# Kernel optimization log

Hardware: AMD Instinct MI355X
Metric: run time of the kernel (lower is better)

## Reference

```python
import jax, jax.numpy as jnp
import numpy as np

B, N, D = 128, 64, 20
H, WM = 256, 4
CAUG = D + 1                      # time-augmented path channels
SIG = CAUG + CAUG * (CAUG - 1) // 2   # depth-2 log-signature channels = 231
C = SIG + 1                       # time-augmented control channels = 232
EPS = 1e-5


def _ln(x, g, b):
    m = jnp.mean(x, -1, keepdims=True)
    v = jnp.var(x, -1, keepdims=True)
    return (x - m) * jax.lax.rsqrt(v + EPS) * g + b


def setup_inputs():
    key = jax.random.key(0)
    ks = jax.random.split(key, 12)
    w = lambda k, s: (jax.random.normal(k, s) * 0.02).astype(jnp.float32)
    z = lambda s: jnp.zeros(s, jnp.float32)
    o = lambda s: jnp.ones(s, jnp.float32)
    return dict(
        x=jax.random.normal(ks[0], (B, N, D), jnp.float32),
        hW1=w(ks[1], (D, H)), hb1=z(H), hW2=w(ks[2], (H, H)), hb2=z(H),
        fW1=w(ks[3], (H, WM * H)), fb1=z(WM * H), g1=o(WM * H), be1=z(WM * H),
        fW2=w(ks[4], (WM * H, H)), fb2=z(H), g2=o(H), be2=z(H),
        fW3=w(ks[5], (H, H)), fb3=z(H),
        fW4=w(ks[6], (H, H * C)), fb4=z(H * C),
        yW1=w(ks[7], (H, H // 2)), yb1=z(H // 2), yW2=w(ks[8], (H // 2, 1)), yb2=z(1),
        zW1=w(ks[9], (H, H)), zb1=z(H), zW2=w(ks[10], (H, D)), zb2=z(D),
        sg=o(SIG), sb=z(SIG),
    )


def _forward(x, hW1, hb1, hW2, hb2, fW1, fb1, g1, be1, fW2, fb2, g2, be2,
             fW3, fb3, fW4, fb4, yW1, yb1, yW2, yb2, zW1, zb1, zW2, zb2, sg, sb):
    t = jnp.linspace(0.0, 1.0, N).astype(x.dtype)
    # --- depth-2 streamed log-signature of time-augmented path, basepoint 0 ---
    p = jnp.concatenate([jnp.broadcast_to(t[None, :, None], (B, N, 1)), x], -1)  # (B,N,CAUG)
    prev = jnp.concatenate([jnp.zeros((B, 1, CAUG), x.dtype), p[:, :-1]], 1)
    d = p - prev                                          # piecewise-linear segment increments
    term = prev[..., :, None] * d[..., None, :] - d[..., :, None] * prev[..., None, :]
    levy = 0.5 * jnp.cumsum(term, axis=1)                 # Levy areas, (B,N,CAUG,CAUG)
    iu, ju = np.triu_indices(CAUG, 1)
    logsig = jnp.concatenate([p, levy[:, :, iu, ju]], -1)  # level-1 + level-2 log-sig, (B,N,SIG)
    logsig = _ln(logsig, sg, sb)                          # sig_norm
    # --- natural cubic spline of time-augmented control ---
    y = jnp.concatenate([jnp.broadcast_to(t[None, :, None], (B, N, 1)), logsig], -1)  # (B,N,C)
    h = 1.0 / (N - 1)
    A = np.zeros((N, N), np.float32)
    A[0, 0] = A[-1, -1] = 1.0
    for i in range(1, N - 1):
        A[i, i - 1] = h / 6.0
        A[i, i] = 2.0 * h / 3.0
        A[i, i + 1] = h / 6.0
    rhs = jnp.concatenate([jnp.zeros((B, 1, C), y.dtype),
                           (y[:, 2:] - 2.0 * y[:, 1:-1] + y[:, :-2]) / h,
                           jnp.zeros((B, 1, C), y.dtype)], 1)
    M = jnp.linalg.solve(jnp.asarray(A), rhs.transpose(1, 0, 2).reshape(N, B * C))
    M = M.reshape(N, B, C).transpose(1, 0, 2)             # natural-spline second derivatives
    dy = (y[:, 1:] - y[:, :-1]) / h
    d_knot = dy - (h / 6.0) * (2.0 * M[:, :-1] + M[:, 1:])   # dX/dt at left knots, (B,N-1,C)
    d_mid = dy + (h / 24.0) * (M[:, :-1] - M[:, 1:])         # dX/dt at segment midpoints
    # --- initial hidden state ---
    h0 = jax.nn.relu(x[:, 0] @ hW1 + hb1) @ hW2 + hb2

    def vf(zz):  # RDEFunc MLP -> (B,H,C)
        a = jax.nn.relu(_ln(zz @ fW1 + fb1, g1, be1))
        a = jax.nn.relu(_ln(a @ fW2 + fb2, g2, be2))
        a = jax.nn.relu(a @ fW3 + fb3)
        return (a @ fW4 + fb4).reshape(B, H, C)

    def g(zz, dX):
        return jnp.einsum('bhc,bc->bh', vf(zz), dX)

    def step(zz, dd):  # explicit midpoint step of dz = F(z) dX/dt dt
        dk, dm = dd
        k1 = g(zz, dk)
        zn = zz + h * g(zz + 0.5 * h * k1, dm)
        return zn, zn

    _, hs = jax.lax.scan(step, h0, (d_knot.transpose(1, 0, 2), d_mid.transpose(1, 0, 2)))
    hT = hs[-1]                                            # terminal hidden (return_path=False)
    Y = jax.nn.relu(hT @ yW1 + yb1) @ yW2 + yb2
    Z = jax.nn.relu(hT @ zW1 + zb1) @ zW2 + zb2
    return Y, Z, hT


def reference(x, hW1, hb1, hW2, hb2, fW1, fb1, g1, be1, fW2, fb2, g2, be2,
              fW3, fb3, fW4, fb4, yW1, yb1, yW2, yb2, zW1, zb1, zW2, zb2, sg, sb):
    return _forward(x, hW1, hb1, hW2, hb2, fW1, fb1, g1, be1, fW2, fb2, g2, be2,
                    fW3, fb3, fW4, fb4, yW1, yb1, yW2, yb2, zW1, zb1, zW2, zb2, sg, sb)
```

## Files before the change

### kernel.cpp

```cpp
#include <hip/hip_runtime.h>

#define B 128
#define N 64
#define D 20
#define H 256
#define WMH 1024
#define CAUG 21
#define SIG 231
#define C 232
#define CP 240
#define KA 288
#define NSEG 63
#define NPH 126
#define HSTEP (1.0f/63.0f)
#define EPS 1e-5f

typedef __attribute__((ext_vector_type(8))) short short8;
typedef __attribute__((ext_vector_type(4))) float f32x4;
typedef __attribute__((ext_vector_type(4))) unsigned int uint4v;
typedef __attribute__((ext_vector_type(2))) int int2v;
typedef __attribute__((ext_vector_type(4))) int int4v;
typedef unsigned int uint;

__device__ inline short f2bf(float f) {
  uint u = __float_as_uint(f);
  uint r = (u + 0x7fffu + ((u >> 16) & 1u)) >> 16;
  return (short)r;
}
__device__ inline float bf2f(short h) {
  return __uint_as_float(((uint)(unsigned short)h) << 16);
}
#define MFMA16(a, b, c) __builtin_amdgcn_mfma_f32_16x16x32_bf16((a), (b), (c), 0, 0, 0)

__device__ inline void cstoreu(uint* p, uint v) {
  __hip_atomic_store(p, v, __ATOMIC_RELAXED, __HIP_MEMORY_SCOPE_AGENT);
}
__device__ inline void cstoref(float* p, float v) {
  __hip_atomic_store(p, v, __ATOMIC_RELAXED, __HIP_MEMORY_SCOPE_AGENT);
}
__device__ inline void cstorei(int* p, int v) {
  __hip_atomic_store(p, v, __ATOMIC_RELAXED, __HIP_MEMORY_SCOPE_AGENT);
}

#define CLOAD8(r0,r1,r2,r3,r4,r5,r6,r7,addr)                                   \
  asm volatile("global_load_dwordx4 %0, %8, off sc0 sc1\n\t"                   \
               "global_load_dwordx4 %1, %8, off offset:16 sc0 sc1\n\t"         \
               "global_load_dwordx4 %2, %8, off offset:128 sc0 sc1\n\t"        \
               "global_load_dwordx4 %3, %8, off offset:144 sc0 sc1\n\t"        \
               "global_load_dwordx4 %4, %8, off offset:256 sc0 sc1\n\t"        \
               "global_load_dwordx4 %5, %8, off offset:272 sc0 sc1\n\t"        \
               "global_load_dwordx4 %6, %8, off offset:384 sc0 sc1\n\t"        \
               "global_load_dwordx4 %7, %8, off offset:400 sc0 sc1\n\t"        \
               "s_waitcnt vmcnt(0)"                                            \
               : "=&v"(r0), "=&v"(r1), "=&v"(r2), "=&v"(r3),                   \
                 "=&v"(r4), "=&v"(r5), "=&v"(r6), "=&v"(r7)                    \
               : "v"(addr)                                                     \
               : "memory")

#define CLOAD2(r0,r1,addr)                                                     \
  asm volatile("global_load_dwordx4 %0, %2, off sc0 sc1\n\t"                   \
               "global_load_dwordx4 %1, %2, off offset:16 sc0 sc1\n\t"         \
               "s_waitcnt vmcnt(0)"                                            \
               : "=&v"(r0), "=&v"(r1) : "v"(addr) : "memory")

#define CLOAD9(r0,r1,r2,r3,r4,r5,r6,r7,r8,a0,a1,a2,a3,a4,a5,a6,a7,a8)          \
  asm volatile("global_load_dwordx4 %0, %9, off sc0 sc1\n\t"                   \
               "global_load_dwordx4 %1, %10, off sc0 sc1\n\t"                  \
               "global_load_dwordx4 %2, %11, off sc0 sc1\n\t"                  \
               "global_load_dwordx4 %3, %12, off sc0 sc1\n\t"                  \
               "global_load_dwordx4 %4, %13, off sc0 sc1\n\t"                  \
               "global_load_dwordx4 %5, %14, off sc0 sc1\n\t"                  \
               "global_load_dwordx4 %6, %15, off sc0 sc1\n\t"                  \
               "global_load_dwordx4 %7, %16, off sc0 sc1\n\t"                  \
               "global_load_dwordx4 %8, %17, off sc0 sc1\n\t"                  \
               "s_waitcnt vmcnt(0)"                                            \
               : "=&v"(r0), "=&v"(r1), "=&v"(r2), "=&v"(r3), "=&v"(r4),        \
                 "=&v"(r5), "=&v"(r6), "=&v"(r7), "=&v"(r8)                    \
               : "v"(a0), "v"(a1), "v"(a2), "v"(a3), "v"(a4), "v"(a5),         \
                 "v"(a6), "v"(a7), "v"(a8)                                     \
               : "memory")

__device__ inline void post(int* w, int v) {
  __builtin_amdgcn_fence(__ATOMIC_RELEASE, "workgroup");
  __syncthreads();
  if (threadIdx.x == 0) cstorei(w, v);
}
__device__ inline void poll16(const int* f, int tgt) {
  if (threadIdx.x < 64) {
    const int* p = f + (threadIdx.x & 15);
    for (;;) {
      int v;
      asm volatile("global_load_dword %0, %1, off sc0 sc1\n\ts_waitcnt vmcnt(0)"
                   : "=v"(v) : "v"(p) : "memory");
      if (__all(v >= tgt)) break;
      __builtin_amdgcn_s_sleep(1);
    }
  }
  __builtin_amdgcn_fence(__ATOMIC_ACQUIRE, "workgroup");
  __syncthreads();
}
__device__ inline void poll128(const int* f, int tgt) {
  if (threadIdx.x < 64) {
    const int* p = f + threadIdx.x * 2;
    for (;;) {
      int2v v;
      asm volatile("global_load_dwordx2 %0, %1, off sc0 sc1\n\ts_waitcnt vmcnt(0)"
                   : "=v"(v) : "v"(p) : "memory");
      if (__all(v[0] >= tgt && v[1] >= tgt)) break;
      __builtin_amdgcn_s_sleep(1);
    }
  }
  __builtin_amdgcn_fence(__ATOMIC_ACQUIRE, "workgroup");
  __syncthreads();
}
__device__ inline void poll256(const int* f, int tgt) {
  if (threadIdx.x < 64) {
    const int* p = f + threadIdx.x * 4;
    for (;;) {
      int4v v;
      asm volatile("global_load_dwordx4 %0, %1, off sc0 sc1\n\ts_waitcnt vmcnt(0)"
                   : "=v"(v) : "v"(p) : "memory");
      if (__all(v[0] >= tgt && v[1] >= tgt && v[2] >= tgt && v[3] >= tgt)) break;
      __builtin_amdgcn_s_sleep(1);
    }
  }
  __builtin_amdgcn_fence(__ATOMIC_ACQUIRE, "workgroup");
  __syncthreads();
}

__device__ inline void unpk(uint4v a, uint4v b, short8& ah, short8& al) {
#pragma unroll
  for (int e = 0; e < 4; e++) {
    ah[e]     = (short)(a[e] >> 16); al[e]     = (short)(a[e] & 0xffffu);
    ah[4 + e] = (short)(b[e] >> 16); al[4 + e] = (short)(b[e] & 0xffffu);
  }
}

__global__ __launch_bounds__(256) void k_logsig(const float* __restrict__ x,
                                                const float* __restrict__ sg,
                                                const float* __restrict__ sb,
                                                float* __restrict__ y) {
  __shared__ float yb[N][C];
  int b = blockIdx.x, tid = threadIdx.x;
  for (int ii = tid; ii < N * CAUG; ii += 256) {
    int n = ii / CAUG, j = ii % CAUG;
    float v = (j == 0) ? (n * (1.0f / 63.0f)) : x[(b * N + n) * D + (j - 1)];
    yb[n][1 + j] = v;
  }
  __syncthreads();
  if (tid < 210) {
    int i = 0, rem = tid;
    while (rem >= (CAUG - 1) - i) { rem -= (CAUG - 1) - i; i++; }
    int j = i + 1 + rem;
    float acc = 0.f, pi_prev = 0.f, pj_prev = 0.f;
    for (int n = 0; n < N; n++) {
      float pi = yb[n][1 + i], pj = yb[n][1 + j];
      float di = pi - pi_prev, dj = pj - pj_prev;
      acc += 0.5f * (pi_prev * dj - di * pj_prev);
      yb[n][1 + CAUG + tid] = acc;
      pi_prev = pi; pj_prev = pj;
    }
  }
  __syncthreads();
  int w = tid >> 6, l = tid & 63;
  for (int n = w; n < N; n += 4) {
    float s1 = 0.f, s2 = 0.f;
    for (int s = l; s < SIG; s += 64) { float v = yb[n][1 + s]; s1 += v; s2 += v * v; }
    for (int off = 32; off > 0; off >>= 1) { s1 += __shfl_down(s1, off); s2 += __shfl_down(s2, off); }
    s1 = __shfl(s1, 0); s2 = __shfl(s2, 0);
    float mean = s1 * (1.0f / SIG);
    float var  = s2 * (1.0f / SIG) - mean * mean;
    float rs = rsqrtf(var + EPS);
    float* yrow = y + ((size_t)b * N + n) * C;
    if (l == 0) yrow[0] = n * (1.0f / 63.0f);
    for (int s = l; s < SIG; s += 64)
      yrow[1 + s] = (yb[n][1 + s] - mean) * rs * sg[s] + sb[s];
  }
}

__global__ __launch_bounds__(256) void k_spline(const float* __restrict__ y,
                                                float* __restrict__ dknot,
                                                float* __restrict__ dmid) {
  __shared__ float yb[N * C];
  __shared__ float cp_s[62], id_s[62];
  int b = blockIdx.x, tid = threadIdx.x;
  for (int ii = tid; ii < N * C; ii += 256) yb[ii] = y[(size_t)b * N * C + ii];
  if (tid == 0) {
    const float a = HSTEP / 6.f, bb = 2.f * HSTEP / 3.f;
    float id0 = 1.f / bb; id_s[0] = id0; cp_s[0] = a * id0;
    for (int j = 1; j < 62; j++) {
      float den = bb - a * cp_s[j - 1];
      float idj = 1.f / den; id_s[j] = idj; cp_s[j] = a * idj;
    }
  }
  __syncthreads();
  int c = tid;
  if (c >= 232 && c < CP) {
    for (int n = 0; n < NSEG; n++) {
      dknot[((size_t)n * B + b) * CP + c] = 0.f;
      dmid [((size_t)n * B + b) * CP + c] = 0.f;
    }
  } else if (c < 232) {
    const float a = HSTEP / 6.f;
    float dp[62];
    dp[0] = (yb[2 * C + c] - 2.f * yb[1 * C + c] + yb[0 * C + c]) * 63.0f * id_s[0];
#pragma unroll
    for (int j = 1; j < 62; j++) {
      float rj = (yb[(j + 2) * C + c] - 2.f * yb[(j + 1) * C + c] + yb[j * C + c]) * 63.0f;
      dp[j] = (rj - a * dp[j - 1]) * id_s[j];
    }
#pragma unroll
    for (int j = 60; j >= 0; j--) dp[j] -= cp_s[j] * dp[j + 1];
#pragma unroll
    for (int n = 0; n < NSEG; n++) {
      float Mn  = (n == 0)  ? 0.f : dp[n - 1];
      float Mn1 = (n == 62) ? 0.f : dp[n];
      float dy = (yb[(n + 1) * C + c] - yb[n * C + c]) * 63.0f;
      dknot[((size_t)n * B + b) * CP + c] = dy - (HSTEP / 6.f)  * (2.f * Mn + Mn1);
      dmid [((size_t)n * B + b) * CP + c] = dy + (HSTEP / 24.f) * (Mn - Mn1);
    }
  }
}

__global__ __launch_bounds__(256) void k_h0(const float* __restrict__ x,
                                            const float* __restrict__ hW1,
                                            const float* __restrict__ hb1,
                                            const float* __restrict__ hW2,
                                            const float* __restrict__ hb2,
                                            float* __restrict__ z,
                                            uint* __restrict__ Xu) {
  __shared__ float r[H];
  int b = blockIdx.x, tid = threadIdx.x;
  float s = hb1[tid];
#pragma unroll
  for (int d = 0; d < D; d++) s += x[(size_t)(b * N) * D + d] * hW1[d * H + tid];
  r[tid] = fmaxf(s, 0.f);
  __syncthreads();
  float s2 = hb2[tid];
  for (int k = 0; k < H; k++) s2 += r[k] * hW2[k * H + tid];
  z[b * H + tid] = s2;
  short hi = f2bf(s2);
  short lo = f2bf(s2 - bf2f(hi));
  Xu[b * H + tid] = ((uint)(unsigned short)hi << 16) | (unsigned short)lo;
}

__global__ __launch_bounds__(256) void k_prep_t(const float* __restrict__ fW4,
                                                short* __restrict__ W4T) {
  __shared__ float tile[64][65];
  int m0 = blockIdx.x * 64, k0 = blockIdx.y * 64;
  int lane = threadIdx.x & 63, wr = threadIdx.x >> 6;
#pragma unroll
  for (int j = 0; j < 16; j++) {
    int kk = wr * 16 + j;
    tile[kk][lane] = fW4[(size_t)(k0 + kk) * 59392 + m0 + lane];
  }
  __syncthreads();
#pragma unroll
  for (int j = 0; j < 16; j++) {
    int mloc = wr * 16 + j;
    int m = m0 + mloc;
    int hh = m / 232, cc = m - hh * 232;
    W4T[((size_t)hh * CP + cc) * KA + k0 + lane] = f2bf(tile[lane][mloc]);
  }
}

__global__ __launch_bounds__(256) void k_prep_pad(const float* __restrict__ fb4,
                                                  short* __restrict__ W4T) {
  int idx = blockIdx.x * 256 + threadIdx.x;
  const int partA = 61440 * 32;
  if (idx < partA) {
    int row = idx >> 5, j = idx & 31;
    int hh = row / CP, cc = row - hh * CP;
    short v = 0;
    if (j == 0 && cc < 232) v = f2bf(fb4[hh * 232 + cc]);
    W4T[(size_t)row * KA + 256 + j] = v;
  } else {
    int t = idx - partA;
    int k = t & 255; t >>= 8;
    int cc = 232 + (t & 7); int hh = t >> 3;
    W4T[((size_t)hh * CP + cc) * KA + k] = 0;
  }
}

__global__ __launch_bounds__(256) void k_prep_wt(const float* __restrict__ in,
                                                 short* __restrict__ out,
                                                 int K, int Nn) {
  __shared__ float tile[64][65];
  int n0 = blockIdx.x * 64, k0 = blockIdx.y * 64;
  int lane = threadIdx.x & 63, wr = threadIdx.x >> 6;
#pragma unroll
  for (int j = 0; j < 16; j++) {
    int kk = wr * 16 + j;
    tile[kk][lane] = in[(size_t)(k0 + kk) * Nn + n0 + lane];
  }
  __syncthreads();
#pragma unroll
  for (int j = 0; j < 16; j++) {
    int nl = wr * 16 + j;
    out[(size_t)(n0 + nl) * K + k0 + lane] = f2bf(tile[lane][nl]);
  }
}

__global__ __launch_bounds__(128) void k_prep_t3pad(short* __restrict__ t3aug) {
  int r = threadIdx.x;
  if (r < 128) {
    int base = ((r >> 4) * 9 + 8) * 64 + (r & 15);
#pragma unroll
    for (int q = 0; q < 4; q++)
#pragma unroll
      for (int j = 0; j < 8; j++)
        t3aug[(size_t)(base + q * 16) * 8 + j] = (q == 0 && j == 0) ? (short)0x3F80 : (short)0;
  }
}

__global__ __launch_bounds__(256) void k_prep_zero(int* __restrict__ p, int n) {
  int i = blockIdx.x * 256 + threadIdx.x;
  if (i < n) p[i] = 0;
}

__global__ __launch_bounds__(512, 1) void k_scan(
    const short* __restrict__ W1T, const float* __restrict__ fb1,
    const float* __restrict__ g1,  const float* __restrict__ be1,
    const short* __restrict__ W2T, const float* __restrict__ fb2,
    const float* __restrict__ g2,  const float* __restrict__ be2,
    const short* __restrict__ W3T, const float* __restrict__ fb3,
    const short* __restrict__ W4T,
    const float* __restrict__ dknot, const float* __restrict__ dmid,
    float* __restrict__ z, uint* __restrict__ Xu, uint* __restrict__ t3u,
    float* __restrict__ T1, float* __restrict__ T2,
    int* __restrict__ flags) {
  const int blk = blockIdx.x;
  const int tid = threadIdx.x;
  const int wave = tid >> 6, lane = tid & 63;
  const int lm = lane & 15, q = lane >> 4;
  const int m = (blk & 127) >> 4;
  const int n = blk & 15;
  const int ks = wave >> 2, nwt = wave & 3;

  __shared__ short t3s[B * KA];
  __shared__ float red2[8][256];
  __shared__ float red4[8][128];
  __shared__ float zcol[128];
  __shared__ float g1s[WMH], be1s[WMH];
  __shared__ float g2s[H], be2s[H];
  __shared__ float fb1s[64];
  __shared__ float fb2s[16], fb3s[16];

  int* eS1 = flags;
  int* eS2 = flags + 128;
  int* eS3 = flags + 256;
  int* eS4 = flags + 384;

  const int nts = (wave < 7) ? 2 : 1;
  const int nt0 = wave * 2;
  short8 bfr[2][9];
  for (int t = 0; t < nts; t++) {
    const short* wp = W4T + ((size_t)blk * CP + (nt0 + t) * 16 + lm) * KA + q * 8;
#pragma unroll
    for (int kc = 0; kc < 9; kc++)
      bfr[t][kc] = *(const short8*)(wp + kc * 32);
  }
  short8 w1f[4], w2f[4], w3f;
  if (blk < 128) {
    const short* p1 = W1T + ((size_t)(n * 64 + nwt * 16 + lm)) * H + ks * 128 + q * 8;
#pragma unroll
    for (int kc = 0; kc < 4; kc++) w1f[kc] = *(const short8*)(p1 + kc * 32);
    const short* p2 = W2T + ((size_t)(n * 16 + lm)) * WMH + wave * 128 + q * 8;
#pragma unroll
    for (int kc = 0; kc < 4; kc++) w2f[kc] = *(const short8*)(p2 + kc * 32);
    w3f = *(const short8*)(W3T + ((size_t)(n * 16 + lm)) * H + wave * 32 + q * 8);
  }
  for (int i = tid; i < WMH; i += 512) { g1s[i] = g1[i]; be1s[i] = be1[i]; }
  for (int i = tid; i < H; i += 512)   { g2s[i] = g2[i]; be2s[i] = be2[i]; }
  if (tid < 64) fb1s[tid] = fb1[n * 64 + tid];
  if (tid < 16) { fb2s[tid] = fb2[n * 16 + tid]; fb3s[tid] = fb3[n * 16 + tid]; }
  if (tid < 128) zcol[tid] = z[(size_t)tid * H + blk];
  __syncthreads();

#pragma unroll 1
  for (int p = 0; p < NPH; p++) {
    const int seg = p >> 1, pm = p & 1;
    const float* dX = (pm ? dmid : dknot) + (size_t)seg * B * CP;
    const float scale = pm ? HSTEP : 0.5f * HSTEP;

    if (blk < 128) {
      if (p) poll256(eS4, p);
      const uint* xp = Xu + (size_t)(m * 16 + lm) * H + ks * 128 + q * 8;
      uint4v xv[8];
      CLOAD8(xv[0], xv[1], xv[2], xv[3], xv[4], xv[5], xv[6], xv[7], xp);
      {
        f32x4 acc = {0.f, 0.f, 0.f, 0.f};
#pragma unroll
        for (int kc = 0; kc < 4; kc++) {
          short8 ah, al;
          unpk(xv[kc * 2], xv[kc * 2 + 1], ah, al);
          acc = MFMA16(ah, w1f[kc], acc);
          acc = MFMA16(al, w1f[kc], acc);
        }
#pragma unroll
        for (int r = 0; r < 4; r++) red2[wave][(q * 4 + r) * 16 + lm] = acc[r];
      }
      __syncthreads();
      if (wave < 4) {
        int col = n * 64 + wave * 16 + lm;
        float fb = fb1s[wave * 16 + lm];
#pragma unroll
        for (int r = 0; r < 4; r++) {
          int idx = (q * 4 + r) * 16 + lm;
          float v = red2[wave][idx] + red2[wave + 4][idx] + fb;
          cstoref(T1 + (size_t)(m * 16 + q * 4 + r) * WMH + col, v);
        }
      }
      post(eS1 + m * 16 + n, p + 1);

      poll16(eS1 + m * 16, p + 1);
      const float* tp = T1 + (size_t)(m * 16 + lm) * WMH + wave * 128 + q * 8;
      uint4v yv[8];
      CLOAD8(yv[0], yv[1], yv[2], yv[3], yv[4], yv[5], yv[6], yv[7], tp);
      {
        float s = 0.f, ss = 0.f;
#pragma unroll
        for (int i = 0; i < 8; i++)
#pragma unroll
          for (int e = 0; e < 4; e++) {
            float v = __uint_as_float(yv[i][e]);
            s += v; ss += v * v;
          }
        s += __shfl_xor(s, 16); ss += __shfl_xor(ss, 16);
        s += __shfl_xor(s, 32); ss += __shfl_xor(ss, 32);
        if (q == 0) { red2[wave][lm] = s; red2[wave][16 + lm] = ss; }
        __syncthreads();
        float S = 0.f, SS = 0.f;
#pragma unroll
        for (int w = 0; w < 8; w++) { S += red2[w][lm]; SS += red2[w][16 + lm]; }
        float mean = S * (1.f / WMH);
        float var  = SS * (1.f / WMH) - mean * mean;
        float rsv  = rsqrtf(var + EPS);
        __syncthreads();
        f32x4 acc = {0.f, 0.f, 0.f, 0.f};
#pragma unroll
        for (int kc = 0; kc < 4; kc++) {
          int kg = wave * 128 + kc * 32 + q * 8;
          short8 ah, al;
#pragma unroll
          for (int jj = 0; jj < 8; jj++) {
            float v = __uint_as_float(yv[kc * 2 + (jj >> 2)][jj & 3]);
            float a = fmaxf((v - mean) * rsv * g1s[kg + jj] + be1s[kg + jj], 0.f);
            short hi = f2bf(a);
            ah[jj] = hi;
            al[jj] = f2bf(a - bf2f(hi));
          }
          acc = MFMA16(ah, w2f[kc], acc);
          acc = MFMA16(al, w2f[kc], acc);
        }
#pragma unroll
        for (int r = 0; r < 4; r++) red2[wave][(q * 4 + r) * 16 + lm] = acc[r];
      }
      __syncthreads();
      if (tid < 256) {
        int ri = tid >> 4, ci = tid & 15;
        float v = fb2s[ci];
#pragma unroll
        for (int w = 0; w < 8; w++) v += red2[w][tid];
        cstoref(T2 + (size_t)(m * 16 + ri) * H + n * 16 + ci, v);
      }
      post(eS2 + m * 16 + n, p + 1);

      poll16(eS2 + m * 16, p + 1);
      const float* t2p = T2 + (size_t)(m * 16 + lm) * H + wave * 32 + q * 8;
      uint4v u0, u1;
      CLOAD2(u0, u1, t2p);
      {
        float s = 0.f, ss = 0.f;
#pragma unroll
        for (int e = 0; e < 4; e++) {
          float v0 = __uint_as_float(u0[e]), v1 = __uint_as_float(u1[e]);
          s += v0 + v1; ss += v0 * v0 + v1 * v1;
        }
        s += __shfl_xor(s, 16); ss += __shfl_xor(ss, 16);
        s += __shfl_xor(s, 32); ss += __shfl_xor(ss, 32);
        if (q == 0) { red2[wave][lm] = s; red2[wave][16 + lm] = ss; }
        __syncthreads();
        float S = 0.f, SS = 0.f;
#pragma unroll
        for (int w = 0; w < 8; w++) { S += red2[w][lm]; SS += red2[w][16 + lm]; }
        float mean = S * (1.f / H);
        float var  = SS * (1.f / H) - mean * mean;
        float rsv  = rsqrtf(var + EPS);
        __syncthreads();
        int kg = wave * 32 + q * 8;
        short8 ah, al;
#pragma unroll
        for (int jj = 0; jj < 8; jj++) {
          float v = __uint_as_float((jj < 4 ? u0[jj & 3] : u1[jj & 3]));
          float a = fmaxf((v - mean) * rsv * g2s[kg + jj] + be2s[kg + jj], 0.f);
          short hi = f2bf(a);
          ah[jj] = hi;
          al[jj] = f2bf(a - bf2f(hi));
        }
        f32x4 acc = {0.f, 0.f, 0.f, 0.f};
        acc = MFMA16(ah, w3f, acc);
        acc = MFMA16(al, w3f, acc);
#pragma unroll
        for (int r = 0; r < 4; r++) red2[wave][(q * 4 + r) * 16 + lm] = acc[r];
      }
      __syncthreads();
      if (tid < 256) {
        int ri = tid >> 4, ci = tid & 15;
        float v = fb3s[ci];
#pragma unroll
        for (int w = 0; w < 8; w++) v += red2[w][tid];
        v = fmaxf(v, 0.f);
        float vo = __shfl_xor(v, 1);
        if ((ci & 1) == 0) {
          int kglob = n * 16 + ci;
          int d = (m * 9 + (kglob >> 5)) * 64 + ((kglob >> 3) & 3) * 16 + ri;
          uint u = ((uint)(unsigned short)f2bf(vo) << 16)
                 | (unsigned short)f2bf(v);
          cstoreu(t3u + d * 4 + ((kglob & 7) >> 1), u);
        }
      }
      post(eS3 + m * 16 + n, p + 1);
    }

    {
      poll128(eS3, p + 1);
      {
        const uint* tb = t3u + tid * 4;
        uint4v r0, r1, r2, r3, r4, r5, r6, r7, r8;
        CLOAD9(r0, r1, r2, r3, r4, r5, r6, r7, r8,
               tb, tb + 2048, tb + 4096, tb + 6144, tb + 8192,
               tb + 10240, tb + 12288, tb + 14336, tb + 16384);
        *(uint4v*)(t3s + (size_t)(0 * 2048 + tid * 4) * 2) = r0;
        *(uint4v*)(t3s + (size_t)(1 * 2048 + tid * 4) * 2) = r1;
        *(uint4v*)(t3s + (size_t)(2 * 2048 + tid * 4) * 2) = r2;
        *(uint4v*)(t3s + (size_t)(3 * 2048 + tid * 4) * 2) = r3;
        *(uint4v*)(t3s + (size_t)(4 * 2048 + tid * 4) * 2) = r4;
        *(uint4v*)(t3s + (size_t)(5 * 2048 + tid * 4) * 2) = r5;
        *(uint4v*)(t3s + (size_t)(6 * 2048 + tid * 4) * 2) = r6;
        *(uint4v*)(t3s + (size_t)(7 * 2048 + tid * 4) * 2) = r7;
        *(uint4v*)(t3s + (size_t)(8 * 2048 + tid * 4) * 2) = r8;
      }
      __syncthreads();
      for (int mm = 0; mm < 8; mm++) {
        short8 afr[9];
#pragma unroll
        for (int kc = 0; kc < 9; kc++)
          afr[kc] = *(const short8*)(t3s + (size_t)((mm * 9 + kc) * 64 + lane) * 8);
        f32x4 acc0 = {0.f, 0.f, 0.f, 0.f}, acc1 = {0.f, 0.f, 0.f, 0.f};
#pragma unroll
        for (int kc = 0; kc < 9; kc++) {
          acc0 = MFMA16(afr[kc], bfr[0][kc], acc0);
          if (nts > 1) acc1 = MFMA16(afr[kc], bfr[1][kc], acc1);
        }
        float part[4];
#pragma unroll
        for (int r = 0; r < 4; r++) {
          int row = mm * 16 + q * 4 + r;
          float pv = acc0[r] * dX[(size_t)row * CP + nt0 * 16 + lm];
          if (nts > 1) pv += acc1[r] * dX[(size_t)row * CP + (nt0 + 1) * 16 + lm];
          part[r] = pv;
        }
#pragma unroll
        for (int r = 0; r < 4; r++) {
          part[r] += __shfl_xor(part[r], 1);
          part[r] += __shfl_xor(part[r], 2);
          part[r] += __shfl_xor(part[r], 4);
          part[r] += __shfl_xor(part[r], 8);
        }
        if (lm == 0) {
#pragma unroll
          for (int r = 0; r < 4; r++) red4[wave][mm * 16 + q * 4 + r] = part[r];
        }
      }
      __syncthreads();
      if (tid < 128) {
        int row = tid;
        float s = 0.f;
#pragma unroll
        for (int w = 0; w < 8; w++) s += red4[w][row];
        float zo = zcol[row] + scale * s;
        if (pm) zcol[row] = zo;
        if (p == NPH - 1) z[(size_t)row * H + blk] = zo;
        short hi = f2bf(zo);
        short lo = f2bf(zo - bf2f(hi));
        cstoreu(Xu + (size_t)row * H + blk,
                ((uint)(unsigned short)hi << 16) | (unsigned short)lo);
      }
      post(eS4 + blk, p + 1);
    }
  }
}

__global__ __launch_bounds__(256) void k_final(const float* __restrict__ z,
    const float* __restrict__ yW1, const float* __restrict__ yb1,
    const float* __restrict__ yW2, const float* __restrict__ yb2,
    const float* __restrict__ zW1, const float* __restrict__ zb1,
    const float* __restrict__ zW2, const float* __restrict__ zb2,
    float* __restrict__ out) {
  __shared__ float ht[H];
  __shared__ float ry[128];
  __shared__ float rz[H];
  int b = blockIdx.x, tid = threadIdx.x;
  ht[tid] = z[(size_t)b * H + tid];
  __syncthreads();
  if (tid < 128) {
    float s = yb1[tid];
    for (int k = 0; k < H; k++) s += ht[k] * yW1[k * 128 + tid];
    ry[tid] = fmaxf(s, 0.f);
  }
  {
    float s = zb1[tid];
    for (int k = 0; k < H; k++) s += ht[k] * zW1[k * H + tid];
    rz[tid] = fmaxf(s, 0.f);
  }
  __syncthreads();
  if (tid < 64) {
    float sv = ry[tid] * yW2[tid] + ry[tid + 64] * yW2[tid + 64];
    for (int off = 32; off > 0; off >>= 1) sv += __shfl_down(sv, off);
    if (tid == 0) out[b] = sv + yb2[0];
  }
  if (tid < D) {
    float s = zb2[tid];
    for (int k = 0; k < H; k++) s += rz[k] * zW2[k * D + tid];
    out[B + b * D + tid] = s;
  }
  out[B + B * D + (size_t)b * H + tid] = ht[tid];
}

extern "C" void kernel_launch(void* const* d_in, const int* in_sizes, int n_in,
                              void* d_out, int out_size, void* d_ws, size_t ws_size,
                              hipStream_t stream) {
  const float* x   = (const float*)d_in[0];
  const float* hW1 = (const float*)d_in[1];
  const float* hb1 = (const float*)d_in[2];
  const float* hW2 = (const float*)d_in[3];
  const float* hb2 = (const float*)d_in[4];
  const float* fW1 = (const float*)d_in[5];
  const float* fb1 = (const float*)d_in[6];
  const float* g1  = (const float*)d_in[7];
  const float* be1 = (const float*)d_in[8];
  const float* fW2 = (const float*)d_in[9];
  const float* fb2 = (const float*)d_in[10];
  const float* g2  = (const float*)d_in[11];
  const float* be2 = (const float*)d_in[12];
  const float* fW3 = (const float*)d_in[13];
  const float* fb3 = (const float*)d_in[14];
  const float* fW4 = (const float*)d_in[15];
  const float* fb4 = (const float*)d_in[16];
  const float* yW1 = (const float*)d_in[17];
  const float* yb1 = (const float*)d_in[18];
  const float* yW2 = (const float*)d_in[19];
  const float* yb2 = (const float*)d_in[20];
  const float* zW1 = (const float*)d_in[21];
  const float* zb1 = (const float*)d_in[22];
  const float* zW2 = (const float*)d_in[23];
  const float* zb2 = (const float*)d_in[24];
  const float* sg  = (const float*)d_in[25];
  const float* sb  = (const float*)d_in[26];

  float* ws     = (float*)d_ws;
  float* dknot  = ws;
  float* dmid   = dknot + (size_t)NSEG * B * CP;
  float* z      = dmid + (size_t)NSEG * B * CP;
  float* T1     = z + B * H;
  float* T2     = T1 + B * WMH;
  uint* Xu      = (uint*)(T2 + B * H);
  uint* t3u     = Xu + B * H;
  int* flags    = (int*)(t3u + B * KA / 2);
  short* w1T    = (short*)(flags + 1024);
  short* w2T    = w1T + H * WMH;
  short* w3T    = w2T + H * WMH;
  short* W4T    = w3T + H * H;
  float* y      = (float*)W4T;

  hipLaunchKernelGGL(k_logsig, dim3(B), dim3(256), 0, stream, x, sg, sb, y);
  hipLaunchKernelGGL(k_spline, dim3(B), dim3(256), 0, stream, y, dknot, dmid);
  hipLaunchKernelGGL(k_h0,     dim3(B), dim3(256), 0, stream, x, hW1, hb1, hW2, hb2, z, Xu);
  hipLaunchKernelGGL(k_prep_t,   dim3(928, 4), dim3(256), 0, stream, fW4, W4T);
  hipLaunchKernelGGL(k_prep_pad, dim3(9728),   dim3(256), 0, stream, fb4, W4T);
  hipLaunchKernelGGL(k_prep_wt,  dim3(16, 4),  dim3(256), 0, stream, fW1, w1T, H, WMH);
  hipLaunchKernelGGL(k_prep_wt,  dim3(4, 16),  dim3(256), 0, stream, fW2, w2T, WMH, H);
  hipLaunchKernelGGL(k_prep_wt,  dim3(4, 4),   dim3(256), 0, stream, fW3, w3T, H, H);
  hipLaunchKernelGGL(k_prep_t3pad, dim3(1), dim3(128), 0, stream, (short*)t3u);
  hipLaunchKernelGGL(k_prep_zero, dim3(4), dim3(256), 0, stream, flags, 1024);

  void* args[] = {
    (void*)&w1T, (void*)&fb1, (void*)&g1, (void*)&be1,
    (void*)&w2T, (void*)&fb2, (void*)&g2, (void*)&be2,
    (void*)&w3T, (void*)&fb3, (void*)&W4T,
    (void*)&dknot, (void*)&dmid,
    (void*)&z, (void*)&Xu, (void*)&t3u,
    (void*)&T1, (void*)&T2, (void*)&flags
  };
  hipLaunchCooperativeKernel((const void*)k_scan, dim3(256), dim3(512), args, 0, stream);

  hipLaunchKernelGGL(k_final, dim3(B), dim3(256), 0, stream, z,
                     yW1, yb1, yW2, yb2, zW1, zb1, zW2, zb2, (float*)d_out);
}
```

Measured before the change: 4.611 ms.

## Stagger global access order across blocks and stage X through shared memory

```diff
diff --git a/kernel.cpp b/kernel.cpp
--- a/kernel.cpp
+++ b/kernel.cpp
@@ -62,6 +62,12 @@
                "global_load_dwordx4 %1, %2, off offset:16 sc0 sc1\n\t"         \
                "s_waitcnt vmcnt(0)"                                            \
                : "=&v"(r0), "=&v"(r1) : "v"(addr) : "memory")
+
+#define CLOADB2(r0,r1,a0,a1)                                                   \
+  asm volatile("global_load_dwordx4 %0, %2, off sc0 sc1\n\t"                   \
+               "global_load_dwordx4 %1, %3, off sc0 sc1\n\t"                   \
+               "s_waitcnt vmcnt(0)"                                            \
+               : "=&v"(r0), "=&v"(r1) : "v"(a0), "v"(a1) : "memory")
 
 #define CLOAD9(r0,r1,r2,r3,r4,r5,r6,r7,r8,a0,a1,a2,a3,a4,a5,a6,a7,a8)          \
   asm volatile("global_load_dwordx4 %0, %9, off sc0 sc1\n\t"                   \
@@ -336,6 +342,8 @@
   const int m = (blk & 127) >> 4;
   const int n = blk & 15;
   const int ks = wave >> 2, nwt = wave & 3;
+  const int wv2 = (wave + n) & 7;
+  const int wv3 = (wave + n) & 7;
 
   __shared__ short t3s[B * KA];
   __shared__ float red2[8][256];
@@ -345,6 +353,7 @@
   __shared__ float g2s[H], be2s[H];
   __shared__ float fb1s[64];
   __shared__ float fb2s[16], fb3s[16];
+  __shared__ uint xs[16 * 260];
 
   int* eS1 = flags;
   int* eS2 = flags + 128;
@@ -365,10 +374,10 @@
     const short* p1 = W1T + ((size_t)(n * 64 + nwt * 16 + lm)) * H + ks * 128 + q * 8;
 #pragma unroll
     for (int kc = 0; kc < 4; kc++) w1f[kc] = *(const short8*)(p1 + kc * 32);
-    const short* p2 = W2T + ((size_t)(n * 16 + lm)) * WMH + wave * 128 + q * 8;
+    const short* p2 = W2T + ((size_t)(n * 16 + lm)) * WMH + wv2 * 128 + q * 8;
 #pragma unroll
     for (int kc = 0; kc < 4; kc++) w2f[kc] = *(const short8*)(p2 + kc * 32);
-    w3f = *(const short8*)(W3T + ((size_t)(n * 16 + lm)) * H + wave * 32 + q * 8);
+    w3f = *(const short8*)(W3T + ((size_t)(n * 16 + lm)) * H + wv3 * 32 + q * 8);
   }
   for (int i = tid; i < WMH; i += 512) { g1s[i] = g1[i]; be1s[i] = be1[i]; }
   for (int i = tid; i < H; i += 512)   { g2s[i] = g2[i]; be2s[i] = be2[i]; }
@@ -385,15 +394,24 @@
 
     if (blk < 128) {
       if (p) poll256(eS4, p);
-      const uint* xp = Xu + (size_t)(m * 16 + lm) * H + ks * 128 + q * 8;
-      uint4v xv[8];
-      CLOAD8(xv[0], xv[1], xv[2], xv[3], xv[4], xv[5], xv[6], xv[7], xp);
+      {
+        const uint* xsrc = Xu + (size_t)(m * 16) * H;
+        int j0 = tid * 4, j1 = (tid + 512) * 4;
+        uint4v v0, v1;
+        CLOADB2(v0, v1, xsrc + j0, xsrc + j1);
+        *(uint4v*)&xs[(j0 >> 8) * 260 + (j0 & 255)] = v0;
+        *(uint4v*)&xs[(j1 >> 8) * 260 + (j1 & 255)] = v1;
+      }
+      __syncthreads();
       {
         f32x4 acc = {0.f, 0.f, 0.f, 0.f};
+        const int xb = lm * 260 + ks * 128 + q * 8;
 #pragma unroll
         for (int kc = 0; kc < 4; kc++) {
+          uint4v a = *(const uint4v*)&xs[xb + kc * 32];
+          uint4v b = *(const uint4v*)&xs[xb + kc * 32 + 4];
           short8 ah, al;
-          unpk(xv[kc * 2], xv[kc * 2 + 1], ah, al);
+          unpk(a, b, ah, al);
           acc = MFMA16(ah, w1f[kc], acc);
           acc = MFMA16(al, w1f[kc], acc);
         }
@@ -414,7 +432,7 @@
       post(eS1 + m * 16 + n, p + 1);
 
       poll16(eS1 + m * 16, p + 1);
-      const float* tp = T1 + (size_t)(m * 16 + lm) * WMH + wave * 128 + q * 8;
+      const float* tp = T1 + (size_t)(m * 16 + lm) * WMH + wv2 * 128 + q * 8;
       uint4v yv[8];
       CLOAD8(yv[0], yv[1], yv[2], yv[3], yv[4], yv[5], yv[6], yv[7], tp);
       {
@@ -440,7 +458,7 @@
         f32x4 acc = {0.f, 0.f, 0.f, 0.f};
 #pragma unroll
         for (int kc = 0; kc < 4; kc++) {
-          int kg = wave * 128 + kc * 32 + q * 8;
+          int kg = wv2 * 128 + kc * 32 + q * 8;
           short8 ah, al;
 #pragma unroll
           for (int jj = 0; jj < 8; jj++) {
@@ -467,7 +485,7 @@
       post(eS2 + m * 16 + n, p + 1);
 
       poll16(eS2 + m * 16, p + 1);
-      const float* t2p = T2 + (size_t)(m * 16 + lm) * H + wave * 32 + q * 8;
+      const float* t2p = T2 + (size_t)(m * 16 + lm) * H + wv3 * 32 + q * 8;
       uint4v u0, u1;
       CLOAD2(u0, u1, t2p);
       {
@@ -488,7 +506,7 @@
         float var  = SS * (1.f / H) - mean * mean;
         float rsv  = rsqrtf(var + EPS);
         __syncthreads();
-        int kg = wave * 32 + q * 8;
+        int kg = wv3 * 32 + q * 8;
         short8 ah, al;
 #pragma unroll
         for (int jj = 0; jj < 8; jj++) {
@@ -521,25 +539,50 @@
         }
       }
       post(eS3 + m * 16 + n, p + 1);
+    } else {
+      if (p + 1 < NPH) {
+        const int seg2 = (p + 1) >> 1, pm2 = (p + 1) & 1;
+        const float* dX2 = (pm2 ? dmid : dknot) + (size_t)seg2 * B * CP;
+        int i0 = tid * 64;
+        if (i0 > B * CP - 64) i0 = B * CP - 64;
+        int i1 = i0 + 32;
+        float t0, t1;
+        asm volatile("global_load_dword %0, %2, off\n\t"
+                     "global_load_dword %1, %3, off\n\t"
+                     "s_waitcnt vmcnt(0)"
+                     : "=&v"(t0), "=&v"(t1)
+                     : "v"(dX2 + i0), "v"(dX2 + i1) : "memory");
+        asm volatile("" :: "v"(t0), "v"(t1));
+      }
     }
 
     {
       poll128(eS3, p + 1);
       {
+        int s0 = blk % 9;
+        int s1 = s0 + 1 >= 9 ? s0 + 1 - 9 : s0 + 1;
+        int s2 = s1 + 1 >= 9 ? s1 + 1 - 9 : s1 + 1;
+        int s3 = s2 + 1 >= 9 ? s2 + 1 - 9 : s2 + 1;
+        int s4 = s3 + 1 >= 9 ? s3 + 1 - 9 : s3 + 1;
+        int s5 = s4 + 1 >= 9 ? s4 + 1 - 9 : s4 + 1;
+        int s6 = s5 + 1 >= 9 ? s5 + 1 - 9 : s5 + 1;
+        int s7 = s6 + 1 >= 9 ? s6 + 1 - 9 : s6 + 1;
+        int s8 = s7 + 1 >= 9 ? s7 + 1 - 9 : s7 + 1;
         const uint* tb = t3u + tid * 4;
         uint4v r0, r1, r2, r3, r4, r5, r6, r7, r8;
         CLOAD9(r0, r1, r2, r3, r4, r5, r6, r7, r8,
-               tb, tb + 2048, tb + 4096, tb + 6144, tb + 8192,
-               tb + 10240, tb + 12288, tb + 14336, tb + 16384);
-        *(uint4v*)(t3s + (size_t)(0 * 2048 + tid * 4) * 2) = r0;
-        *(uint4v*)(t3s + (size_t)(1 * 2048 + tid * 4) * 2) = r1;
-        *(uint4v*)(t3s + (size_t)(2 * 2048 + tid * 4) * 2) = r2;
-        *(uint4v*)(t3s + (size_t)(3 * 2048 + tid * 4) * 2) = r3;
-        *(uint4v*)(t3s + (size_t)(4 * 2048 + tid * 4) * 2) = r4;
-        *(uint4v*)(t3s + (size_t)(5 * 2048 + tid * 4) * 2) = r5;
-        *(uint4v*)(t3s + (size_t)(6 * 2048 + tid * 4) * 2) = r6;
-        *(uint4v*)(t3s + (size_t)(7 * 2048 + tid * 4) * 2) = r7;
-        *(uint4v*)(t3s + (size_t)(8 * 2048 + tid * 4) * 2) = r8;
+               tb + s0 * 2048, tb + s1 * 2048, tb + s2 * 2048,
+               tb + s3 * 2048, tb + s4 * 2048, tb + s5 * 2048,
+               tb + s6 * 2048, tb + s7 * 2048, tb + s8 * 2048);
+        *(uint4v*)(t3s + (size_t)s0 * 4096 + tid * 8) = r0;
+        *(uint4v*)(t3s + (size_t)s1 * 4096 + tid * 8) = r1;
+        *(uint4v*)(t3s + (size_t)s2 * 4096 + tid * 8) = r2;
+        *(uint4v*)(t3s + (size_t)s3 * 4096 + tid * 8) = r3;
+        *(uint4v*)(t3s + (size_t)s4 * 4096 + tid * 8) = r4;
+        *(uint4v*)(t3s + (size_t)s5 * 4096 + tid * 8) = r5;
+        *(uint4v*)(t3s + (size_t)s6 * 4096 + tid * 8) = r6;
+        *(uint4v*)(t3s + (size_t)s7 * 4096 + tid * 8) = r7;
+        *(uint4v*)(t3s + (size_t)s8 * 4096 + tid * 8) = r8;
       }
       __syncthreads();
       for (int mm = 0; mm < 8; mm++) {
```

Measured after the change: 3.787 ms. -17.9%, faster.
